# Optimization experiments

Measured on AMD Instinct MI355X. Metric: run time of the kernel, lower is better.

The kernel has to match this reference:

```python
import jax, jax.numpy as jnp
import numpy as np

EPS = 1e-3  # keras LayerNormalization default epsilon


def layer_norm(x, gamma, beta):
    mu = jnp.mean(x, axis=-1, keepdims=True)
    var = jnp.var(x, axis=-1, keepdims=True)
    return (x - mu) * jax.lax.rsqrt(var + EPS) * gamma + beta


def setup_inputs() -> dict:
    key = jax.random.key(0)
    ks = jax.random.split(key, 16)
    B, S, D = 8, 2048, 1024          # batch, seq, input_size
    P = 2 * D                        # up-projection dim (proj_factor=2)
    H = 1024                         # hidden = head_size(64) * num_heads(16)
    s = 0.02
    inp = {
        "x": jax.random.normal(ks[0], (B, S, D), jnp.float32),
        "ln1_g": jnp.ones((D,), jnp.float32),
        "ln1_b": jnp.zeros((D,), jnp.float32),
        "W_up": jax.random.normal(ks[1], (D, P), jnp.float32) * s,
        "b_up": jnp.zeros((P,), jnp.float32),
        "W_adj": jax.random.normal(ks[2], (P, H), jnp.float32) * s,
        "b_adj": jnp.zeros((H,), jnp.float32),
        "W_q": jax.random.normal(ks[3], (H, H), jnp.float32) * s,
        "b_q": jnp.zeros((H,), jnp.float32),
        "W_k": jax.random.normal(ks[4], (H, H), jnp.float32) * s,
        "b_k": jnp.zeros((H,), jnp.float32),
        "W_v": jax.random.normal(ks[5], (H, H), jnp.float32) * s,
        "b_v": jnp.zeros((H,), jnp.float32),
        "W_i": jax.random.normal(ks[6], (H, H), jnp.float32) * s,
        "b_i": jnp.zeros((H,), jnp.float32),
        "W_f": jax.random.normal(ks[7], (H, H), jnp.float32) * s,
        "b_f": jnp.zeros((H,), jnp.float32),
        "W_o": jax.random.normal(ks[8], (H, H), jnp.float32) * s,
        "b_o": jnp.zeros((H,), jnp.float32),
        "ln2_g": jnp.ones((H,), jnp.float32),
        "ln2_b": jnpos if False else jnp.zeros((H,), jnp.float32),
        "W_down": jax.random.normal(ks[9], (H, D), jnp.float32) * s,
        "b_down": jnp.zeros((D,), jnp.float32),
    }
    return inp


def reference(x, ln1_g, ln1_b, W_up, b_up, W_adj, b_adj,
              W_q, b_q, W_k, b_k, W_v, b_v,
              W_i, b_i, W_f, b_f, W_o, b_o,
              ln2_g, ln2_b, W_down, b_down):
    head_size = 64
    x_norm = layer_norm(x, ln1_g, ln1_b)
    x_up = x_norm @ W_up + b_up                      # [B,S,2D]
    x_adj = x_up @ W_adj + b_adj                     # [B,S,H]
    # BlockDiagonal layers: each block is a Dense over the FULL input,
    # concatenated -> equivalent to one [H,H] matmul with concatenated weights.
    q = x_adj @ W_q + b_q
    k = (x_adj @ W_k + b_k) / (head_size ** 0.5)
    v = x_adj @ W_v + b_v
    i_t = x_adj @ W_i + b_i
    f_t = x_adj @ W_f + b_f
    o = jax.nn.sigmoid(x_adj @ W_o + b_o)
    m_t = jnp.maximum(f_t, i_t)
    f = jnp.exp(f_t - m_t)                           # (i = exp(i_t - m_t) unused downstream)
    c_t = f * v * k
    h_t = o * (c_t * q) / jnp.maximum(jnp.abs(k * q), 1.0)
    out = layer_norm(h_t, ln2_g, ln2_b) * jax.nn.sigmoid(x_adj)
    out = out @ W_down + b_down
    return out + x
```

## Files before the change

kernel.cpp:

```cpp
#include <hip/hip_runtime.h>


typedef unsigned short u16;
typedef __attribute__((ext_vector_type(4))) unsigned short u16x4;
typedef __attribute__((ext_vector_type(8))) unsigned short u16x8;
typedef __attribute__((ext_vector_type(8))) __bf16 bf16x8;
typedef __attribute__((ext_vector_type(4))) float f32x4;

__device__ __forceinline__ float bf2f(u16 u) {
    union { unsigned int i; float f; } c; c.i = ((unsigned int)u) << 16; return c.f;
}
__device__ __forceinline__ u16 f2bf(float f) {
    union { float f; unsigned int i; } c; c.f = f;
    unsigned int lsb = (c.i >> 16) & 1u;
    c.i += 0x7fffu + lsb;
    return (u16)(c.i >> 16);
}
__device__ __forceinline__ float sigmoidf(float z) {
    return 1.0f / (1.0f + __expf(-z));
}

#define GLDS16(gp, lp)                                                        \
    __builtin_amdgcn_global_load_lds(                                         \
        (__attribute__((address_space(1))) void*)(void*)(gp),                 \
        (__attribute__((address_space(3))) void*)(lp), 16, 0, 0)

#define BM 128
#define BN 128
#define BK 32

template <int MODE>
__global__ __launch_bounds__(256) void gemm_bt(
    const u16* __restrict__ A, const u16* __restrict__ Bt,
    const float* __restrict__ bias, const float* __restrict__ resid,
    void* __restrict__ out, int M, int N, int K, float scale)
{
    __shared__ __align__(16) u16 As[2 * BM * BK];
    __shared__ __align__(16) u16 Bs[2 * BN * BK];

    const int tid  = threadIdx.x;
    const int lane = tid & 63;
    const int wave = tid >> 6;
    const int l15  = lane & 15;
    const int quad = lane >> 4;

    const long bm = (long)blockIdx.y * BM;
    const long bn = (long)blockIdx.x * BN;
    const int  wm = (wave >> 1) * 64;
    const int  wn = (wave & 1) * 64;

    f32x4 acc[4][4] = {};

    const int  r0 = tid >> 2;
    const int  ck = (((tid & 3) ^ ((tid >> 3) & 3)) * 8);
    const u16* ga0 = A  + (bm + r0) * (long)K + ck;
    const u16* gb0 = Bt + (bn + r0) * (long)K + ck;
    const int  ldst = wave * 512;

    auto stage = [&](int t_, int b_) {
        const long kof = (long)t_ * BK;
        u16* dA = &As[b_ * (BM * BK) + ldst];
        u16* dB = &Bs[b_ * (BN * BK) + ldst];
        GLDS16(ga0 + kof, dA);
        GLDS16(ga0 + kof + 64 * (long)K, dA + 2048);
        GLDS16(gb0 + kof, dB);
        GLDS16(gb0 + kof + 64 * (long)K, dB + 2048);
    };

    const int q8s = (quad ^ ((l15 >> 1) & 3)) * 8;
    const int nk  = K / BK;

    stage(0, 0);
    stage(1, 1);

    for (int t = 0; t < nk; ++t) {
        const int cur = t & 1;
        if (t + 1 < nk) asm volatile("s_waitcnt vmcnt(4)" ::: "memory");
        else            asm volatile("s_waitcnt vmcnt(0)" ::: "memory");
        __builtin_amdgcn_s_barrier();

        bf16x8 af[4], bfr[4];
#pragma unroll
        for (int t4 = 0; t4 < 4; ++t4) {
            af[t4]  = *(const bf16x8*)&As[cur * (BM * BK) + (wm + t4 * 16 + l15) * BK + q8s];
            bfr[t4] = *(const bf16x8*)&Bs[cur * (BN * BK) + (wn + t4 * 16 + l15) * BK + q8s];
        }
        asm volatile("s_waitcnt lgkmcnt(0)" ::: "memory");
        __builtin_amdgcn_s_barrier();
        if (t + 2 < nk) stage(t + 2, cur);

        __builtin_amdgcn_s_setprio(1);
#pragma unroll
        for (int mt = 0; mt < 4; ++mt)
#pragma unroll
            for (int nt = 0; nt < 4; ++nt)
                acc[mt][nt] = __builtin_amdgcn_mfma_f32_16x16x32_bf16(
                    af[mt], bfr[nt], acc[mt][nt], 0, 0, 0);
        __builtin_amdgcn_s_setprio(0);
    }

#pragma unroll
    for (int nt = 0; nt < 4; ++nt) {
        const long n  = bn + wn + nt * 16 + l15;
        const float bv = (MODE == 2) ? 0.0f : bias[n];
#pragma unroll
        for (int mt = 0; mt < 4; ++mt) {
            const long m0 = bm + wm + mt * 16 + quad * 4;
#pragma unroll
            for (int r = 0; r < 4; ++r) {
                const long idx = (m0 + r) * N + n;
                const float val = (acc[mt][nt][r] + bv) * scale;
                if (MODE == 1) ((float*)out)[idx] = val + resid[idx];
                else           ((u16*)out)[idx] = f2bf(val);
            }
        }
    }
}

__global__ __launch_bounds__(256) void gemm_gates(
    const u16* __restrict__ A, const u16* __restrict__ Wcat,
    const float* __restrict__ bq_, const float* __restrict__ bk_,
    const float* __restrict__ bv_, const float* __restrict__ bi_,
    const float* __restrict__ bf_, const float* __restrict__ bo_,
    u16* __restrict__ ht, int M, int N, int K)
{
    __shared__ __align__(16) u16 As[2 * 128 * 64];
    __shared__ __align__(16) u16 Bs[2 * 6 * 32 * 64];

    const int tid  = threadIdx.x;
    const int lane = tid & 63;
    const int wave = tid >> 6;
    const int l15  = lane & 15;
    const int quad = lane >> 4;

    const long bm = (long)blockIdx.y * 128;
    const long bn = (long)blockIdx.x * 32;

    f32x4 acc[6][4] = {};

    const int  rr = lane >> 3;
    const int  ck = (((lane & 7) ^ rr) * 8);

    const u16* gaj[4];
    int lAo[4];
#pragma unroll
    for (int j = 0; j < 4; ++j) {
        const int c = wave * 4 + j;
        gaj[j] = A + (bm + c * 8 + rr) * (long)K + ck;
        lAo[j] = c * 512;
    }
    const u16* gbj[6];
    int lBo[6];
#pragma unroll
    for (int j = 0; j < 6; ++j) {
        const int c = wave * 6 + j;
        const int g = c >> 2;
        const int r = (c & 3) * 8 + rr;
        gbj[j] = Wcat + ((long)g * 1024 + bn + r) * (long)K + ck;
        lBo[j] = c * 512;
    }

    auto stage = [&](int t_, int b_) {
        const long kof = (long)t_ * 64;
#pragma unroll
        for (int j = 0; j < 4; ++j)
            GLDS16(gaj[j] + kof, &As[b_ * 8192 + lAo[j]]);
#pragma unroll
        for (int j = 0; j < 6; ++j)
            GLDS16(gbj[j] + kof, &Bs[b_ * 12288 + lBo[j]]);
    };

    const int mh = (wave >> 1) * 64;
    const int nb = (wave & 1) * 16;
    const int l7 = l15 & 7;
    const int nk = K >> 6;

    stage(0, 0);
    stage(1, 1);

    for (int t = 0; t < nk; ++t) {
        const int cur = t & 1;
        if (t + 1 < nk) asm volatile("s_waitcnt vmcnt(10)" ::: "memory");
        else            asm volatile("s_waitcnt vmcnt(0)"  ::: "memory");
        __builtin_amdgcn_s_barrier();

        const int ab = cur * 8192;
        const int bb = cur * 12288;

        {
            const int so = (quad ^ l7) * 8;
            bf16x8 af[4];
#pragma unroll
            for (int t4 = 0; t4 < 4; ++t4)
                af[t4] = *(const bf16x8*)&As[ab + (mh + t4 * 16 + l15) * 64 + so];
            __builtin_amdgcn_s_setprio(1);
#pragma unroll
            for (int g = 0; g < 6; ++g) {
                const bf16x8 bfrag =
                    *(const bf16x8*)&Bs[bb + (g * 32 + nb + l15) * 64 + so];
#pragma unroll
                for (int t4 = 0; t4 < 4; ++t4)
                    acc[g][t4] = __builtin_amdgcn_mfma_f32_16x16x32_bf16(
                        af[t4], bfrag, acc[g][t4], 0, 0, 0);
            }
            __builtin_amdgcn_s_setprio(0);
        }
        bf16x8 af1[4], bf1[6];
        {
            const int so = ((4 + quad) ^ l7) * 8;
#pragma unroll
            for (int t4 = 0; t4 < 4; ++t4)
                af1[t4] = *(const bf16x8*)&As[ab + (mh + t4 * 16 + l15) * 64 + so];
#pragma unroll
            for (int g = 0; g < 6; ++g)
                bf1[g] = *(const bf16x8*)&Bs[bb + (g * 32 + nb + l15) * 64 + so];
        }
        asm volatile("s_waitcnt lgkmcnt(0)" ::: "memory");
        __builtin_amdgcn_s_barrier();
        if (t + 2 < nk) stage(t + 2, cur);

        __builtin_amdgcn_s_setprio(1);
#pragma unroll
        for (int g = 0; g < 6; ++g)
#pragma unroll
            for (int t4 = 0; t4 < 4; ++t4)
                acc[g][t4] = __builtin_amdgcn_mfma_f32_16x16x32_bf16(
                    af1[t4], bf1[g], acc[g][t4], 0, 0, 0);
        __builtin_amdgcn_s_setprio(0);
    }

    const long n = bn + nb + l15;
    const float bqn = bq_[n], bkn = bk_[n], bvn = bv_[n];
    const float bin = bi_[n], bfn = bf_[n], bon = bo_[n];
#pragma unroll
    for (int t = 0; t < 4; ++t) {
        const long m0 = bm + mh + t * 16 + quad * 4;
#pragma unroll
        for (int r = 0; r < 4; ++r) {
            const float qf = acc[0][t][r] + bqn;
            const float kf = (acc[1][t][r] + bkn) * 0.125f;
            const float vf = acc[2][t][r] + bvn;
            const float fi = acc[3][t][r] + bin;
            const float ff = acc[4][t][r] + bfn;
            const float osig = sigmoidf(acc[5][t][r] + bon);
            const float mx = fmaxf(ff, fi);
            const float fe = __expf(ff - mx);
            const float ct = fe * vf * kf;
            const float h  = osig * (ct * qf) / fmaxf(fabsf(kf * qf), 1.0f);
            ht[(m0 + r) * N + n] = f2bf(h);
        }
    }
}

__global__ __launch_bounds__(256) void ln_in_kernel(
    const float* __restrict__ x, const float* __restrict__ g,
    const float* __restrict__ b, u16* __restrict__ xn)
{
    const long row = blockIdx.x;
    const int  tid = threadIdx.x;
    const float4 v = ((const float4*)(x + row * 1024))[tid];
    float s  = v.x + v.y + v.z + v.w;
    float s2 = v.x * v.x + v.y * v.y + v.z * v.z + v.w * v.w;
#pragma unroll
    for (int off = 32; off > 0; off >>= 1) {
        s  += __shfl_down(s, off);
        s2 += __shfl_down(s2, off);
    }
    __shared__ float red[8];
    const int wave = tid >> 6;
    if ((tid & 63) == 0) { red[wave] = s; red[4 + wave] = s2; }
    __syncthreads();
    if (tid == 0) {
        const float S  = red[0] + red[1] + red[2] + red[3];
        const float S2 = red[4] + red[5] + red[6] + red[7];
        const float mu = S * (1.0f / 1024.0f);
        const float var = S2 * (1.0f / 1024.0f) - mu * mu;
        red[0] = mu; red[1] = rsqrtf(var + 1e-3f);
    }
    __syncthreads();
    const float mu = red[0], rstd = red[1];
    const int c = tid * 4;
    u16x4 o;
    o.x = f2bf((v.x - mu) * rstd * g[c + 0] + b[c + 0]);
    o.y = f2bf((v.y - mu) * rstd * g[c + 1] + b[c + 1]);
    o.z = f2bf((v.z - mu) * rstd * g[c + 2] + b[c + 2]);
    o.w = f2bf((v.w - mu) * rstd * g[c + 3] + b[c + 3]);
    *(u16x4*)(xn + row * 1024 + c) = o;
}

struct PrepArgs {
    const float *Wadj, *Wq, *Wk, *Wv, *Wi, *Wf, *Wo, *Wdn, *Wup;
    const float *bup, *badj;
    u16 *WadjT, *Wcat, *WdnT, *Wup_bf;
    float *bcomb;
};

__device__ __forceinline__ void do_transpose(
    const float* __restrict__ W, u16* __restrict__ Wt,
    int K, int N, int bx, int by, float (&t)[32][33])
{
    const int tx = threadIdx.x & 31;
    const int ty = threadIdx.x >> 5;
    const long bn = (long)bx * 32;
    const long bk = (long)by * 32;
#pragma unroll
    for (int j = 0; j < 4; ++j)
        t[ty + j * 8][tx] = W[(bk + ty + j * 8) * N + bn + tx];
    __syncthreads();
#pragma unroll
    for (int j = 0; j < 4; ++j)
        Wt[(bn + ty + j * 8) * K + bk + tx] = f2bf(t[tx][ty + j * 8]);
}

__global__ __launch_bounds__(256) void prep_kernel(PrepArgs a)
{
    __shared__ float t[32][33];
    int bid = blockIdx.x;
    if (bid < 2048) {
        do_transpose(a.Wadj, a.WadjT, 2048, 1024, bid & 31, bid >> 5, t);
        return;
    }
    bid -= 2048;
    if (bid < 6144) {
        const int g = bid >> 10, tt = bid & 1023;
        const float* Wg = g == 0 ? a.Wq : g == 1 ? a.Wk : g == 2 ? a.Wv
                        : g == 3 ? a.Wi : g == 4 ? a.Wf : a.Wo;
        do_transpose(Wg, a.Wcat + (long)g * 1024 * 1024, 1024, 1024,
                     tt & 31, tt >> 5, t);
        return;
    }
    bid -= 6144;
    if (bid < 1024) {
        do_transpose(a.Wdn, a.WdnT, 1024, 1024, bid & 31, bid >> 5, t);
        return;
    }
    bid -= 1024;
    if (bid < 2048) {
        const long i = ((long)bid * 256 + threadIdx.x) * 4;
        const float4 v = *(const float4*)(a.Wup + i);
        u16x4 o;
        o.x = f2bf(v.x); o.y = f2bf(v.y); o.z = f2bf(v.z); o.w = f2bf(v.w);
        *(u16x4*)(a.Wup_bf + i) = o;
        return;
    }
    bid -= 2048;
    {
        const int h = bid * 256 + threadIdx.x;
        float s = 0.0f;
#pragma unroll 8
        for (int p = 0; p < 2048; ++p)
            s += a.bup[p] * a.Wadj[(long)p * 1024 + h];
        a.bcomb[h] = s + a.badj[h];
    }
}

__global__ __launch_bounds__(256) void ln2_kernel(
    const u16* __restrict__ ht, const u16* __restrict__ xadj,
    const float* __restrict__ g2, const float* __restrict__ b2,
    u16* __restrict__ y)
{
    const long base = (long)blockIdx.x * 1024;
    const int  tid = threadIdx.x;
    const int  c = tid * 4;
    const u16x4 hv = *(const u16x4*)&ht[base + c];
    const u16x4 xv = *(const u16x4*)&xadj[base + c];

    float h[4];
    float s = 0.0f, s2 = 0.0f;
#pragma unroll
    for (int j = 0; j < 4; ++j) {
        h[j] = bf2f(hv[j]);
        s += h[j]; s2 += h[j] * h[j];
    }
#pragma unroll
    for (int off = 32; off > 0; off >>= 1) {
        s  += __shfl_down(s, off);
        s2 += __shfl_down(s2, off);
    }
    __shared__ float red[8];
    const int wave = tid >> 6;
    if ((tid & 63) == 0) { red[wave] = s; red[4 + wave] = s2; }
    __syncthreads();
    if (tid == 0) {
        const float S  = red[0] + red[1] + red[2] + red[3];
        const float S2 = red[4] + red[5] + red[6] + red[7];
        const float mu = S * (1.0f / 1024.0f);
        const float var = S2 * (1.0f / 1024.0f) - mu * mu;
        red[0] = mu; red[1] = rsqrtf(var + 1e-3f);
    }
    __syncthreads();
    const float mu = red[0], rstd = red[1];
    u16x4 o;
#pragma unroll
    for (int j = 0; j < 4; ++j)
        o[j] = f2bf(((h[j] - mu) * rstd * g2[c + j] + b2[c + j]) * sigmoidf(bf2f(xv[j])));
    *(u16x4*)&y[base + c] = o;
}

extern "C" void kernel_launch(void* const* d_in, const int* in_sizes, int n_in,
                              void* d_out, int out_size, void* d_ws, size_t ws_size,
                              hipStream_t stream)
{
    const float* x    = (const float*)d_in[0];
    const float* g1   = (const float*)d_in[1];
    const float* b1   = (const float*)d_in[2];
    const float* Wup  = (const float*)d_in[3];
    const float* bup  = (const float*)d_in[4];
    const float* Wadj = (const float*)d_in[5];
    const float* badj = (const float*)d_in[6];
    const float* Wq = (const float*)d_in[7];   const float* bq = (const float*)d_in[8];
    const float* Wk = (const float*)d_in[9];   const float* bk = (const float*)d_in[10];
    const float* Wv = (const float*)d_in[11];  const float* bv = (const float*)d_in[12];
    const float* Wi = (const float*)d_in[13];  const float* bi = (const float*)d_in[14];
    const float* Wf = (const float*)d_in[15];  const float* bf = (const float*)d_in[16];
    const float* Wo = (const float*)d_in[17];  const float* bo = (const float*)d_in[18];
    const float* g2 = (const float*)d_in[19];  const float* b2 = (const float*)d_in[20];
    const float* Wdn = (const float*)d_in[21]; const float* bdn = (const float*)d_in[22];

    const int M = 8 * 2048;
    const int D = 1024, P = 2048, H = 1024;

    char* ws = (char*)d_ws;
    const size_t MB = 1024 * 1024;
    u16* xn     = (u16*)(ws + 0);
    u16* htb    = (u16*)(ws + 0);
    u16* yb     = (u16*)(ws + 0);
    u16* WcombT = (u16*)(ws + 32 * MB);
    float* bcomb = (float*)(ws + 36 * MB);
    u16* xadj   = (u16*)(ws + 96 * MB);
    u16* Wup_bf = (u16*)(ws + 128 * MB);
    u16* WadjT  = (u16*)(ws + 132 * MB);
    u16* Wcat   = (u16*)(ws + 136 * MB);
    u16* WdnT   = (u16*)(ws + 148 * MB);

    ln_in_kernel<<<M, 256, 0, stream>>>(x, g1, b1, xn);

    PrepArgs pa;
    pa.Wadj = Wadj; pa.Wq = Wq; pa.Wk = Wk; pa.Wv = Wv; pa.Wi = Wi;
    pa.Wf = Wf; pa.Wo = Wo; pa.Wdn = Wdn; pa.Wup = Wup;
    pa.bup = bup; pa.badj = badj;
    pa.WadjT = WadjT; pa.Wcat = Wcat; pa.WdnT = WdnT; pa.Wup_bf = Wup_bf;
    pa.bcomb = bcomb;
    prep_kernel<<<11268, 256, 0, stream>>>(pa);

    gemm_bt<2><<<dim3(D / BN, H / BM), 256, 0, stream>>>(
        WadjT, Wup_bf, nullptr, nullptr, WcombT, H, D, P, 1.0f);

    gemm_bt<0><<<dim3(H / BN, M / BM), 256, 0, stream>>>(
        xn, WcombT, bcomb, nullptr, xadj, M, H, D, 1.0f);

    gemm_gates<<<dim3(H / 32, M / 128), 256, 0, stream>>>(
        xadj, Wcat, bq, bk, bv, bi, bf, bo, htb, M, H, H);

    ln2_kernel<<<M, 256, 0, stream>>>(htb, xadj, g2, b2, yb);

    gemm_bt<1><<<dim3(D / BN, M / BM), 256, 0, stream>>>(yb, WdnT, bdn, x, (float*)d_out, M, D, H, 1.0f);
}
```

Before: 646.5 us.

## Deepen gates GEMM pipeline to four-stage K=32 ring and split bias fold

The gates GEMM moves from a double-buffered K=64 tile loop to a four-slot ring of K=32 stages with three stages in flight, using a single shared buffer and a new XOR swizzle. The goal is to hide global-load latency better and cut per-iteration register pressure. The s_setprio hints are dropped from both GEMMs. The combined-bias dot product moves out of the prep kernel, where each thread did a serial 2048-long strided loop, into its own block-reduction kernel that reads the transposed bf16 Wadj. That adds a launch and uses a bf16-rounded weight instead of fp32.

```diff
diff --git a/kernel.cpp b/kernel.cpp
--- a/kernel.cpp
+++ b/kernel.cpp
@@ -89,14 +89,12 @@
         __builtin_amdgcn_s_barrier();
         if (t + 2 < nk) stage(t + 2, cur);
 
-        __builtin_amdgcn_s_setprio(1);
 #pragma unroll
         for (int mt = 0; mt < 4; ++mt)
 #pragma unroll
             for (int nt = 0; nt < 4; ++nt)
                 acc[mt][nt] = __builtin_amdgcn_mfma_f32_16x16x32_bf16(
                     af[mt], bfr[nt], acc[mt][nt], 0, 0, 0);
-        __builtin_amdgcn_s_setprio(0);
     }
 
 #pragma unroll
@@ -124,8 +122,7 @@
     const float* __restrict__ bf_, const float* __restrict__ bo_,
     u16* __restrict__ ht, int M, int N, int K)
 {
-    __shared__ __align__(16) u16 As[2 * 128 * 64];
-    __shared__ __align__(16) u16 Bs[2 * 6 * 32 * 64];
+    __shared__ __align__(16) u16 S[4 * 10240];
 
     const int tid  = threadIdx.x;
     const int lane = tid & 63;
@@ -138,95 +135,63 @@
 
     f32x4 acc[6][4] = {};
 
-    const int  rr = lane >> 3;
-    const int  ck = (((lane & 7) ^ rr) * 8);
-
-    const u16* gaj[4];
-    int lAo[4];
-#pragma unroll
-    for (int j = 0; j < 4; ++j) {
-        const int c = wave * 4 + j;
-        gaj[j] = A + (bm + c * 8 + rr) * (long)K + ck;
-        lAo[j] = c * 512;
-    }
-    const u16* gbj[6];
-    int lBo[6];
-#pragma unroll
-    for (int j = 0; j < 6; ++j) {
-        const int c = wave * 6 + j;
-        const int g = c >> 2;
-        const int r = (c & 3) * 8 + rr;
-        gbj[j] = Wcat + ((long)g * 1024 + bn + r) * (long)K + ck;
-        lBo[j] = c * 512;
-    }
-
-    auto stage = [&](int t_, int b_) {
-        const long kof = (long)t_ * 64;
-#pragma unroll
-        for (int j = 0; j < 4; ++j)
-            GLDS16(gaj[j] + kof, &As[b_ * 8192 + lAo[j]]);
-#pragma unroll
-        for (int j = 0; j < 6; ++j)
-            GLDS16(gbj[j] + kof, &Bs[b_ * 12288 + lBo[j]]);
+    const int  r0 = tid >> 2;
+    const int  ck = (((tid & 3) ^ ((tid >> 3) & 3)) * 8);
+    const u16* gA0 = A + (bm + r0) * (long)K + ck;
+    const u16* gB[3];
+#pragma unroll
+    for (int j = 0; j < 3; ++j) {
+        const int r = r0 + 64 * j;
+        const int g = r >> 5;
+        gB[j] = Wcat + ((long)g * 1024 + bn + (r & 31)) * (long)K + ck;
+    }
+    const int ldst = wave * 512;
+
+    auto stage = [&](int h) {
+        u16* hb = &S[(h & 3) * 10240];
+        const long kof = (long)h * 32;
+        GLDS16(gA0 + kof, hb + ldst);
+        GLDS16(gA0 + kof + 64 * (long)K, hb + ldst + 2048);
+        u16* bb = hb + 4096;
+        GLDS16(gB[0] + kof, bb + ldst);
+        GLDS16(gB[1] + kof, bb + ldst + 2048);
+        GLDS16(gB[2] + kof, bb + ldst + 4096);
     };
 
-    const int mh = (wave >> 1) * 64;
-    const int nb = (wave & 1) * 16;
-    const int l7 = l15 & 7;
-    const int nk = K >> 6;
-
-    stage(0, 0);
-    stage(1, 1);
-
-    for (int t = 0; t < nk; ++t) {
-        const int cur = t & 1;
-        if (t + 1 < nk) asm volatile("s_waitcnt vmcnt(10)" ::: "memory");
-        else            asm volatile("s_waitcnt vmcnt(0)"  ::: "memory");
+    const int mh  = (wave >> 1) * 64;
+    const int nb  = (wave & 1) * 16;
+    const int q8s = (quad ^ ((l15 >> 1) & 3)) * 8;
+    const int nh  = K >> 5;
+
+    stage(0); stage(1); stage(2);
+
+    for (int s = 0; s < nh; ++s) {
+        const int rem = nh - 1 - s;
+        if (rem >= 2)      asm volatile("s_waitcnt vmcnt(10)" ::: "memory");
+        else if (rem == 1) asm volatile("s_waitcnt vmcnt(5)"  ::: "memory");
+        else               asm volatile("s_waitcnt vmcnt(0)"  ::: "memory");
         __builtin_amdgcn_s_barrier();
 
-        const int ab = cur * 8192;
-        const int bb = cur * 12288;
-
-        {
-            const int so = (quad ^ l7) * 8;
-            bf16x8 af[4];
-#pragma unroll
-            for (int t4 = 0; t4 < 4; ++t4)
-                af[t4] = *(const bf16x8*)&As[ab + (mh + t4 * 16 + l15) * 64 + so];
-            __builtin_amdgcn_s_setprio(1);
-#pragma unroll
-            for (int g = 0; g < 6; ++g) {
-                const bf16x8 bfrag =
-                    *(const bf16x8*)&Bs[bb + (g * 32 + nb + l15) * 64 + so];
-#pragma unroll
-                for (int t4 = 0; t4 < 4; ++t4)
-                    acc[g][t4] = __builtin_amdgcn_mfma_f32_16x16x32_bf16(
-                        af[t4], bfrag, acc[g][t4], 0, 0, 0);
-            }
-            __builtin_amdgcn_s_setprio(0);
-        }
-        bf16x8 af1[4], bf1[6];
-        {
-            const int so = ((4 + quad) ^ l7) * 8;
-#pragma unroll
-            for (int t4 = 0; t4 < 4; ++t4)
-                af1[t4] = *(const bf16x8*)&As[ab + (mh + t4 * 16 + l15) * 64 + so];
-#pragma unroll
-            for (int g = 0; g < 6; ++g)
-                bf1[g] = *(const bf16x8*)&Bs[bb + (g * 32 + nb + l15) * 64 + so];
-        }
+        const u16* Ab = &S[(s & 3) * 10240];
+        const u16* Bb = Ab + 4096;
+        bf16x8 af[4], bfr[6];
+#pragma unroll
+        for (int t4 = 0; t4 < 4; ++t4)
+            af[t4] = *(const bf16x8*)&Ab[(mh + t4 * 16 + l15) * 32 + q8s];
+#pragma unroll
+        for (int g = 0; g < 6; ++g)
+            bfr[g] = *(const bf16x8*)&Bb[(g * 32 + nb + l15) * 32 + q8s];
+
         asm volatile("s_waitcnt lgkmcnt(0)" ::: "memory");
         __builtin_amdgcn_s_barrier();
-        if (t + 2 < nk) stage(t + 2, cur);
-
-        __builtin_amdgcn_s_setprio(1);
+        if (s + 3 < nh) stage(s + 3);
+
 #pragma unroll
         for (int g = 0; g < 6; ++g)
 #pragma unroll
             for (int t4 = 0; t4 < 4; ++t4)
                 acc[g][t4] = __builtin_amdgcn_mfma_f32_16x16x32_bf16(
-                    af1[t4], bf1[g], acc[g][t4], 0, 0, 0);
-        __builtin_amdgcn_s_setprio(0);
+                    af[t4], bfr[g], acc[g][t4], 0, 0, 0);
     }
 
     const long n = bn + nb + l15;
@@ -290,9 +255,7 @@
 
 struct PrepArgs {
     const float *Wadj, *Wq, *Wk, *Wv, *Wi, *Wf, *Wo, *Wdn, *Wup;
-    const float *bup, *badj;
     u16 *WadjT, *Wcat, *WdnT, *Wup_bf;
-    float *bcomb;
 };
 
 __device__ __forceinline__ void do_transpose(
@@ -335,23 +298,34 @@
         return;
     }
     bid -= 1024;
-    if (bid < 2048) {
+    {
         const long i = ((long)bid * 256 + threadIdx.x) * 4;
         const float4 v = *(const float4*)(a.Wup + i);
         u16x4 o;
         o.x = f2bf(v.x); o.y = f2bf(v.y); o.z = f2bf(v.z); o.w = f2bf(v.w);
         *(u16x4*)(a.Wup_bf + i) = o;
-        return;
-    }
-    bid -= 2048;
-    {
-        const int h = bid * 256 + threadIdx.x;
-        float s = 0.0f;
-#pragma unroll 8
-        for (int p = 0; p < 2048; ++p)
-            s += a.bup[p] * a.Wadj[(long)p * 1024 + h];
-        a.bcomb[h] = s + a.badj[h];
-    }
+    }
+}
+
+__global__ __launch_bounds__(256) void bcomb_kernel(
+    const u16* __restrict__ WadjT, const float* __restrict__ bup,
+    const float* __restrict__ badj, float* __restrict__ bcomb)
+{
+    const long h = blockIdx.x;
+    const int  tid = threadIdx.x;
+    const int  p = tid * 8;
+    const u16x8 w = *(const u16x8*)&WadjT[h * 2048 + p];
+    float s = 0.0f;
+#pragma unroll
+    for (int j = 0; j < 8; ++j) s += bf2f(w[j]) * bup[p + j];
+#pragma unroll
+    for (int off = 32; off > 0; off >>= 1) s += __shfl_down(s, off);
+    __shared__ float red[4];
+    const int wave = tid >> 6;
+    if ((tid & 63) == 0) red[wave] = s;
+    __syncthreads();
+    if (tid == 0)
+        bcomb[h] = red[0] + red[1] + red[2] + red[3] + badj[h];
 }
 
 __global__ __launch_bounds__(256) void ln2_kernel(
@@ -438,10 +412,10 @@
     PrepArgs pa;
     pa.Wadj = Wadj; pa.Wq = Wq; pa.Wk = Wk; pa.Wv = Wv; pa.Wi = Wi;
     pa.Wf = Wf; pa.Wo = Wo; pa.Wdn = Wdn; pa.Wup = Wup;
-    pa.bup = bup; pa.badj = badj;
     pa.WadjT = WadjT; pa.Wcat = Wcat; pa.WdnT = WdnT; pa.Wup_bf = Wup_bf;
-    pa.bcomb = bcomb;
-    prep_kernel<<<11268, 256, 0, stream>>>(pa);
+    prep_kernel<<<11264, 256, 0, stream>>>(pa);
+
+    bcomb_kernel<<<H, 256, 0, stream>>>(WadjT, bup, badj, bcomb);
 
     gemm_bt<2><<<dim3(D / BN, H / BM), 256, 0, stream>>>(
         WadjT, Wup_bf, nullptr, nullptr, WcombT, H, D, P, 1.0f);
```

Result: faster. 580.7 us (-10.2%).

## Remap gates GEMM blocks per XCD, split bias combine kernel, drop setprio

Applied to the files above, without the earlier changes.

The gates GEMM now runs on a 1D grid. Block indices are remapped so that each XCD handles a contiguous range of N-columns and all M-tiles within it, which should let those blocks share weight tiles in that XCD's L2. The bias-combination tail moves out of the prep kernel, where 4 blocks each ran a serial 2048-long loop, into a new kernel with one block per output element that does a wave-level reduction over the bf16 transposed Wadj. The s_setprio hints around the MFMA loops are removed. The bias is now computed from bf16-rounded weights, which slightly changes numerics.

```diff
diff --git a/kernel.cpp b/kernel.cpp
--- a/kernel.cpp
+++ b/kernel.cpp
@@ -89,14 +89,12 @@
         __builtin_amdgcn_s_barrier();
         if (t + 2 < nk) stage(t + 2, cur);
 
-        __builtin_amdgcn_s_setprio(1);
 #pragma unroll
         for (int mt = 0; mt < 4; ++mt)
 #pragma unroll
             for (int nt = 0; nt < 4; ++nt)
                 acc[mt][nt] = __builtin_amdgcn_mfma_f32_16x16x32_bf16(
                     af[mt], bfr[nt], acc[mt][nt], 0, 0, 0);
-        __builtin_amdgcn_s_setprio(0);
     }
 
 #pragma unroll
@@ -133,8 +131,13 @@
     const int l15  = lane & 15;
     const int quad = lane >> 4;
 
-    const long bm = (long)blockIdx.y * 128;
-    const long bn = (long)blockIdx.x * 32;
+    const int nmb = M >> 7;
+    const int cn  = (N >> 5) >> 3;
+    const int lin = blockIdx.x;
+    const int xcd = lin & 7;
+    const int i   = lin >> 3;
+    const long bm = (long)(i % nmb) * 128;
+    const long bn = (long)(xcd * cn + i / nmb) * 32;
 
     f32x4 acc[6][4] = {};
 
@@ -193,7 +196,6 @@
 #pragma unroll
             for (int t4 = 0; t4 < 4; ++t4)
                 af[t4] = *(const bf16x8*)&As[ab + (mh + t4 * 16 + l15) * 64 + so];
-            __builtin_amdgcn_s_setprio(1);
 #pragma unroll
             for (int g = 0; g < 6; ++g) {
                 const bf16x8 bfrag =
@@ -203,7 +205,6 @@
                     acc[g][t4] = __builtin_amdgcn_mfma_f32_16x16x32_bf16(
                         af[t4], bfrag, acc[g][t4], 0, 0, 0);
             }
-            __builtin_amdgcn_s_setprio(0);
         }
         bf16x8 af1[4], bf1[6];
         {
@@ -219,14 +220,12 @@
         __builtin_amdgcn_s_barrier();
         if (t + 2 < nk) stage(t + 2, cur);
 
-        __builtin_amdgcn_s_setprio(1);
 #pragma unroll
         for (int g = 0; g < 6; ++g)
 #pragma unroll
             for (int t4 = 0; t4 < 4; ++t4)
                 acc[g][t4] = __builtin_amdgcn_mfma_f32_16x16x32_bf16(
                     af1[t4], bf1[g], acc[g][t4], 0, 0, 0);
-        __builtin_amdgcn_s_setprio(0);
     }
 
     const long n = bn + nb + l15;
@@ -290,9 +289,7 @@
 
 struct PrepArgs {
     const float *Wadj, *Wq, *Wk, *Wv, *Wi, *Wf, *Wo, *Wdn, *Wup;
-    const float *bup, *badj;
     u16 *WadjT, *Wcat, *WdnT, *Wup_bf;
-    float *bcomb;
 };
 
 __device__ __forceinline__ void do_transpose(
@@ -335,23 +332,34 @@
         return;
     }
     bid -= 1024;
-    if (bid < 2048) {
+    {
         const long i = ((long)bid * 256 + threadIdx.x) * 4;
         const float4 v = *(const float4*)(a.Wup + i);
         u16x4 o;
         o.x = f2bf(v.x); o.y = f2bf(v.y); o.z = f2bf(v.z); o.w = f2bf(v.w);
         *(u16x4*)(a.Wup_bf + i) = o;
-        return;
-    }
-    bid -= 2048;
-    {
-        const int h = bid * 256 + threadIdx.x;
-        float s = 0.0f;
-#pragma unroll 8
-        for (int p = 0; p < 2048; ++p)
-            s += a.bup[p] * a.Wadj[(long)p * 1024 + h];
-        a.bcomb[h] = s + a.badj[h];
-    }
+    }
+}
+
+__global__ __launch_bounds__(256) void bcomb_kernel(
+    const u16* __restrict__ WadjT, const float* __restrict__ bup,
+    const float* __restrict__ badj, float* __restrict__ bcomb)
+{
+    const long h = blockIdx.x;
+    const int  tid = threadIdx.x;
+    const int  p = tid * 8;
+    const u16x8 w = *(const u16x8*)&WadjT[h * 2048 + p];
+    float s = 0.0f;
+#pragma unroll
+    for (int j = 0; j < 8; ++j) s += bf2f(w[j]) * bup[p + j];
+#pragma unroll
+    for (int off = 32; off > 0; off >>= 1) s += __shfl_down(s, off);
+    __shared__ float red[4];
+    const int wave = tid >> 6;
+    if ((tid & 63) == 0) red[wave] = s;
+    __syncthreads();
+    if (tid == 0)
+        bcomb[h] = red[0] + red[1] + red[2] + red[3] + badj[h];
 }
 
 __global__ __launch_bounds__(256) void ln2_kernel(
@@ -438,10 +446,10 @@
     PrepArgs pa;
     pa.Wadj = Wadj; pa.Wq = Wq; pa.Wk = Wk; pa.Wv = Wv; pa.Wi = Wi;
     pa.Wf = Wf; pa.Wo = Wo; pa.Wdn = Wdn; pa.Wup = Wup;
-    pa.bup = bup; pa.badj = badj;
     pa.WadjT = WadjT; pa.Wcat = Wcat; pa.WdnT = WdnT; pa.Wup_bf = Wup_bf;
-    pa.bcomb = bcomb;
-    prep_kernel<<<11268, 256, 0, stream>>>(pa);
+    prep_kernel<<<11264, 256, 0, stream>>>(pa);
+
+    bcomb_kernel<<<H, 256, 0, stream>>>(WadjT, bup, badj, bcomb);
 
     gemm_bt<2><<<dim3(D / BN, H / BM), 256, 0, stream>>>(
         WadjT, Wup_bf, nullptr, nullptr, WcombT, H, D, P, 1.0f);
@@ -449,7 +457,7 @@
     gemm_bt<0><<<dim3(H / BN, M / BM), 256, 0, stream>>>(
         xn, WcombT, bcomb, nullptr, xadj, M, H, D, 1.0f);
 
-    gemm_gates<<<dim3(H / 32, M / 128), 256, 0, stream>>>(
+    gemm_gates<<<(M / 128) * (H / 32), 256, 0, stream>>>(
         xadj, Wcat, bq, bk, bv, bi, bf, bo, htb, M, H, H);
 
     ln2_kernel<<<M, 256, 0, stream>>>(htb, xadj, g2, b2, yb);
```

New measurement: 569.6 us. 11.9% less time.
